# Optimization experiments

Measured on AMD Instinct MI355X. Metric: run time of the kernel, lower is better.

## Reference

```python
import jax, jax.numpy as jnp
import numpy as np

# pywt db4 decomposition filters (dec_lo, dec_hi), length 8
DB4_DEC_LO = np.array([-0.010597401784997278, 0.032883011666982945,
                       0.030841381835986965, -0.18703481171888114,
                       -0.02798376941698385, 0.6308807679295904,
                       0.7148465705525415, 0.23037781330885523], dtype=np.float32)
DB4_DEC_HI = np.array([-0.23037781330885523, 0.7148465705525415,
                       -0.6308807679295904, -0.02798376941698385,
                       0.18703481171888114, 0.030841381835986965,
                       -0.032883011666982945, -0.010597401784997278], dtype=np.float32)
LEVEL = 3


def setup_inputs() -> dict:
    key = jax.random.key(0)
    x = jax.random.normal(key, (64, 32, 4096), dtype=jnp.float32)  # (B, N, T)
    return {"x": x,
            "dec_lo": jnp.asarray(DB4_DEC_LO),
            "dec_hi": jnp.asarray(DB4_DEC_HI)}


def _swt(x, dec_lo, dec_hi, level=LEVEL):
    """Stationary (a trous) wavelet transform, matching ptwt.swt semantics."""
    B, N, T = x.shape
    filt_len = dec_lo.shape[0]
    # ptwt flips the filters so conv1d (correlation) performs true convolution
    filt = jnp.stack([dec_lo[::-1], dec_hi[::-1]], axis=0)[:, None, :]  # (2, 1, L)
    res_lo = x.reshape(B * N, 1, T)
    details = []
    for lvl in range(level):
        dil = 2 ** lvl
        padl = dil * (filt_len // 2 - 1)
        padr = dil * (filt_len // 2)
        padded = jnp.pad(res_lo, ((0, 0), (0, 0), (padl, padr)), mode="wrap")  # circular
        res = jax.lax.conv_general_dilated(
            padded, filt, window_strides=(1,), padding="VALID",
            rhs_dilation=(dil,), dimension_numbers=("NCH", "OIH", "NCH"))  # (BN, 2, T)
        res_lo = res[:, 0:1, :]
        details.append(res[:, 1, :])
    # ptwt ordering: [cA_level, cD_level, ..., cD_1]
    coeffs = [res_lo[:, 0, :]] + details[::-1]
    stacked = jnp.stack(coeffs, axis=1)  # (B*N, level+1, T)
    return stacked.reshape(B, N, level + 1, T).transpose(0, 1, 3, 2)  # (B, N, T, level+1)


def reference(x, dec_lo, dec_hi):
    return _swt(x, dec_lo, dec_hi)
```

## Files before the change

### kernel.cpp

```cpp
#include <hip/hip_runtime.h>

#define TLEN 4096
#define NT 256
#define SEG 1024
#define OFF 24
#define BUFW 1088

typedef float f32x4 __attribute__((ext_vector_type(4)));
typedef float f32x2 __attribute__((ext_vector_type(2)));

__device__ __forceinline__ f32x4 ldv4(const float* p) {
    return *reinterpret_cast<const f32x4*>(p);
}

#define W16(n) ((n) < 4 ? qa[(n)] : (n) < 8 ? qb[(n)-4] : (n) < 12 ? qc[(n)-8] : qd[(n)-12])
#define W20(n) ((n) < 4 ? qa[(n)] : (n) < 8 ? qb[(n)-4] : (n) < 12 ? qc[(n)-8] : (n) < 16 ? qd[(n)-12] : qe[(n)-16])
#define W32(n) ((n) < 4 ? qa[(n)] : (n) < 8 ? qb[(n)-4] : (n) < 12 ? qc[(n)-8] : (n) < 16 ? qd[(n)-12] : \
                (n) < 20 ? qe[(n)-16] : (n) < 24 ? qf[(n)-20] : (n) < 28 ? qg[(n)-24] : qh[(n)-28])

__global__ __launch_bounds__(NT) void swt_db4_l3_kernel(
    const float* __restrict__ x,
    const float* __restrict__ lo_g,
    const float* __restrict__ hi_g,
    float* __restrict__ out)
{
    __shared__ float bufX[BUFW];
    __shared__ float bufY[BUFW];
    __shared__ float pl[4][SEG];

    const int bid = blockIdx.x;
    const int row = bid >> 2;
    const int seg = (bid & 3) << 10;
    const int tid = threadIdx.x;

    f32x2 c[8];
#pragma unroll
    for (int j = 0; j < 8; ++j) { c[j].x = lo_g[j]; c[j].y = hi_g[j]; }

    const float* xr = x + (size_t)row * TLEN;

    {
        int idx = 4 * tid;
        *reinterpret_cast<f32x4*>(&bufX[OFF + idx]) = ldv4(xr + seg + idx);
    }
    if (tid < 49) {
        int u = (tid < 21) ? (tid - 21) : (SEG + tid - 21);
        bufX[OFF + u] = xr[(seg + u) & (TLEN - 1)];
    }
    __syncthreads();

    float d1[4], d2[4], a3[4], d3[4];

    {
        const float* b = &bufX[OFF + 4 * tid - 4];
        f32x4 qa = ldv4(b), qb = ldv4(b + 4), qc = ldv4(b + 8), qd = ldv4(b + 12);
        f32x2 acc[4];
#pragma unroll
        for (int i = 0; i < 4; ++i) { acc[i].x = 0.f; acc[i].y = 0.f; }
#pragma unroll
        for (int j = 0; j < 8; ++j)
#pragma unroll
            for (int i = 0; i < 4; ++i) {
                float v = W16(i + 8 - j);
                f32x2 vv; vv.x = v; vv.y = v;
                acc[i] = __builtin_elementwise_fma(c[j], vv, acc[i]);
            }
        f32x4 av; av.x = acc[0].x; av.y = acc[1].x; av.z = acc[2].x; av.w = acc[3].x;
        *reinterpret_cast<f32x4*>(&bufY[OFF + 4 * tid]) = av;
#pragma unroll
        for (int i = 0; i < 4; ++i) d1[i] = acc[i].y;
    }
    if (tid < 42) {
        int u = (tid < 18) ? (tid - 18) : (SEG + tid - 18);
        const float* s = &bufX[OFF + u];
        float a = 0.f;
#pragma unroll
        for (int j = 0; j < 8; ++j) a = fmaf(c[j].x, s[4 - j], a);
        bufY[OFF + u] = a;
    }
    __syncthreads();

    {
        const float* b = &bufY[OFF + 4 * tid - 8];
        f32x4 qa = ldv4(b), qb = ldv4(b + 4), qc = ldv4(b + 8), qd = ldv4(b + 12), qe = ldv4(b + 16);
        f32x2 acc[4];
#pragma unroll
        for (int i = 0; i < 4; ++i) { acc[i].x = 0.f; acc[i].y = 0.f; }
#pragma unroll
        for (int j = 0; j < 8; ++j)
#pragma unroll
            for (int i = 0; i < 4; ++i) {
                float v = W20(i + 16 - 2 * j);
                f32x2 vv; vv.x = v; vv.y = v;
                acc[i] = __builtin_elementwise_fma(c[j], vv, acc[i]);
            }
        f32x4 av; av.x = acc[0].x; av.y = acc[1].x; av.z = acc[2].x; av.w = acc[3].x;
        *reinterpret_cast<f32x4*>(&bufX[OFF + 4 * tid]) = av;
#pragma unroll
        for (int i = 0; i < 4; ++i) d2[i] = acc[i].y;
    }
    if (tid < 28) {
        int u = (tid < 12) ? (tid - 12) : (SEG + tid - 12);
        const float* s = &bufY[OFF + u];
        float a = 0.f;
#pragma unroll
        for (int j = 0; j < 8; ++j) a = fmaf(c[j].x, s[(4 - j) * 2], a);
        bufX[OFF + u] = a;
    }
    __syncthreads();

    {
        const float* b = &bufX[OFF + 4 * tid - 12];
        f32x4 qa = ldv4(b),      qb = ldv4(b + 4),  qc = ldv4(b + 8),  qd = ldv4(b + 12),
              qe = ldv4(b + 16), qf = ldv4(b + 20), qg = ldv4(b + 24), qh = ldv4(b + 28);
        f32x2 acc[4];
#pragma unroll
        for (int i = 0; i < 4; ++i) { acc[i].x = 0.f; acc[i].y = 0.f; }
#pragma unroll
        for (int j = 0; j < 8; ++j)
#pragma unroll
            for (int i = 0; i < 4; ++i) {
                float v = W32(i + 28 - 4 * j);
                f32x2 vv; vv.x = v; vv.y = v;
                acc[i] = __builtin_elementwise_fma(c[j], vv, acc[i]);
            }
#pragma unroll
        for (int i = 0; i < 4; ++i) { a3[i] = acc[i].x; d3[i] = acc[i].y; }
    }

    {
        f32x4 v0, v1, v2, v3;
        v0.x=a3[0]; v0.y=a3[1]; v0.z=a3[2]; v0.w=a3[3];
        v1.x=d3[0]; v1.y=d3[1]; v1.z=d3[2]; v1.w=d3[3];
        v2.x=d2[0]; v2.y=d2[1]; v2.z=d2[2]; v2.w=d2[3];
        v3.x=d1[0]; v3.y=d1[1]; v3.z=d1[2]; v3.w=d1[3];
        *reinterpret_cast<f32x4*>(&pl[0][4 * tid]) = v0;
        *reinterpret_cast<f32x4*>(&pl[1][4 * tid]) = v1;
        *reinterpret_cast<f32x4*>(&pl[2][4 * tid]) = v2;
        *reinterpret_cast<f32x4*>(&pl[3][4 * tid]) = v3;
    }
    __syncthreads();

    f32x4* outr = reinterpret_cast<f32x4*>(out + (size_t)row * TLEN * 4) + seg;
#pragma unroll
    for (int k = 0; k < 4; ++k) {
        int t = tid + k * NT;
        f32x4 o;
        o.x = pl[0][t];
        o.y = pl[1][t];
        o.z = pl[2][t];
        o.w = pl[3][t];
        outr[t] = o;
    }
}

extern "C" void kernel_launch(void* const* d_in, const int* in_sizes, int n_in,
                              void* d_out, int out_size, void* d_ws, size_t ws_size,
                              hipStream_t stream) {
    const float* x  = (const float*)d_in[0];
    const float* lo = (const float*)d_in[1];
    const float* hi = (const float*)d_in[2];
    float* out = (float*)d_out;

    const int nblocks = 64 * 32 * 4;
    swt_db4_l3_kernel<<<dim3(nblocks), dim3(NT), 0, stream>>>(x, lo, hi, out);
}
```

Measured before the change: 31.56 us.

## Process all four segments per block with prefetch of next segment's input

Each block now handles a whole row, looping over four 1024-sample segments instead of launching one block per segment. The global load for the next segment is issued before the current segment's compute so its latency overlaps the convolution work, and the shared buffers are merged so the output staging area aliases the work buffers. The intent is to hide global-load latency and reduce block launch overhead. The cost is a quarter as many blocks, which lowers parallelism, plus extra barriers per segment that serialize the stages within a block.

```diff
diff --git a/kernel.cpp b/kernel.cpp
--- a/kernel.cpp
+++ b/kernel.cpp
@@ -4,7 +4,8 @@
 #define NT 256
 #define SEG 1024
 #define OFF 24
-#define BUFW 1088
+#define BUFW 2176
+#define NSEGS 4
 
 typedef float f32x4 __attribute__((ext_vector_type(4)));
 typedef float f32x2 __attribute__((ext_vector_type(2)));
@@ -24,13 +25,12 @@
     const float* __restrict__ hi_g,
     float* __restrict__ out)
 {
-    __shared__ float bufX[BUFW];
-    __shared__ float bufY[BUFW];
-    __shared__ float pl[4][SEG];
+    __shared__ float lds[2 * BUFW];
+    float* bufX = lds;
+    float* bufY = lds + BUFW;
+    float* pl   = lds;
 
-    const int bid = blockIdx.x;
-    const int row = bid >> 2;
-    const int seg = (bid & 3) << 10;
+    const int row = blockIdx.x;
     const int tid = threadIdx.x;
 
     f32x2 c[8];
@@ -38,119 +38,133 @@
     for (int j = 0; j < 8; ++j) { c[j].x = lo_g[j]; c[j].y = hi_g[j]; }
 
     const float* xr = x + (size_t)row * TLEN;
+    f32x4* outb = reinterpret_cast<f32x4*>(out + (size_t)row * TLEN * 4);
 
-    {
-        int idx = 4 * tid;
-        *reinterpret_cast<f32x4*>(&bufX[OFF + idx]) = ldv4(xr + seg + idx);
-    }
-    if (tid < 49) {
-        int u = (tid < 21) ? (tid - 21) : (SEG + tid - 21);
-        bufX[OFF + u] = xr[(seg + u) & (TLEN - 1)];
-    }
-    __syncthreads();
+    const int hu = (tid < 21) ? (tid - 21) : (SEG + tid - 21);
 
-    float d1[4], d2[4], a3[4], d3[4];
+    f32x4 xpre = ldv4(xr + 4 * tid);
+    float xh = (tid < 49) ? xr[hu & (TLEN - 1)] : 0.f;
 
-    {
-        const float* b = &bufX[OFF + 4 * tid - 4];
-        f32x4 qa = ldv4(b), qb = ldv4(b + 4), qc = ldv4(b + 8), qd = ldv4(b + 12);
-        f32x2 acc[4];
+    for (int s = 0; s < NSEGS; ++s) {
+        *reinterpret_cast<f32x4*>(&bufX[OFF + 4 * tid]) = xpre;
+        if (tid < 49) bufX[OFF + hu] = xh;
+        __syncthreads();
+
+        f32x4 xnext;
+        float xhn = 0.f;
+        if (s + 1 < NSEGS) {
+            xnext = ldv4(xr + (s + 1) * SEG + 4 * tid);
+            if (tid < 49) xhn = xr[((s + 1) * SEG + hu) & (TLEN - 1)];
+        }
+
+        float d1[4], d2[4], a3[4], d3[4];
+
+        {
+            const float* b = &bufX[OFF + 4 * tid - 4];
+            f32x4 qa = ldv4(b), qb = ldv4(b + 4), qc = ldv4(b + 8), qd = ldv4(b + 12);
+            f32x2 acc[4];
 #pragma unroll
-        for (int i = 0; i < 4; ++i) { acc[i].x = 0.f; acc[i].y = 0.f; }
+            for (int i = 0; i < 4; ++i) { acc[i].x = 0.f; acc[i].y = 0.f; }
 #pragma unroll
-        for (int j = 0; j < 8; ++j)
+            for (int j = 0; j < 8; ++j)
 #pragma unroll
-            for (int i = 0; i < 4; ++i) {
-                float v = W16(i + 8 - j);
-                f32x2 vv; vv.x = v; vv.y = v;
-                acc[i] = __builtin_elementwise_fma(c[j], vv, acc[i]);
-            }
-        f32x4 av; av.x = acc[0].x; av.y = acc[1].x; av.z = acc[2].x; av.w = acc[3].x;
-        *reinterpret_cast<f32x4*>(&bufY[OFF + 4 * tid]) = av;
+                for (int i = 0; i < 4; ++i) {
+                    float v = W16(i + 8 - j);
+                    f32x2 vv; vv.x = v; vv.y = v;
+                    acc[i] = __builtin_elementwise_fma(c[j], vv, acc[i]);
+                }
+            f32x4 av; av.x = acc[0].x; av.y = acc[1].x; av.z = acc[2].x; av.w = acc[3].x;
+            *reinterpret_cast<f32x4*>(&bufY[OFF + 4 * tid]) = av;
 #pragma unroll
-        for (int i = 0; i < 4; ++i) d1[i] = acc[i].y;
-    }
-    if (tid < 42) {
-        int u = (tid < 18) ? (tid - 18) : (SEG + tid - 18);
-        const float* s = &bufX[OFF + u];
-        float a = 0.f;
+            for (int i = 0; i < 4; ++i) d1[i] = acc[i].y;
+        }
+        if (tid < 42) {
+            int u = (tid < 18) ? (tid - 18) : (SEG + tid - 18);
+            const float* sp = &bufX[OFF + u];
+            float a = 0.f;
 #pragma unroll
-        for (int j = 0; j < 8; ++j) a = fmaf(c[j].x, s[4 - j], a);
-        bufY[OFF + u] = a;
-    }
-    __syncthreads();
+            for (int j = 0; j < 8; ++j) a = fmaf(c[j].x, sp[4 - j], a);
+            bufY[OFF + u] = a;
+        }
+        __syncthreads();
 
-    {
-        const float* b = &bufY[OFF + 4 * tid - 8];
-        f32x4 qa = ldv4(b), qb = ldv4(b + 4), qc = ldv4(b + 8), qd = ldv4(b + 12), qe = ldv4(b + 16);
-        f32x2 acc[4];
+        {
+            const float* b = &bufY[OFF + 4 * tid - 8];
+            f32x4 qa = ldv4(b), qb = ldv4(b + 4), qc = ldv4(b + 8), qd = ldv4(b + 12), qe = ldv4(b + 16);
+            f32x2 acc[4];
 #pragma unroll
-        for (int i = 0; i < 4; ++i) { acc[i].x = 0.f; acc[i].y = 0.f; }
+            for (int i = 0; i < 4; ++i) { acc[i].x = 0.f; acc[i].y = 0.f; }
 #pragma unroll
-        for (int j = 0; j < 8; ++j)
+            for (int j = 0; j < 8; ++j)
 #pragma unroll
-            for (int i = 0; i < 4; ++i) {
-                float v = W20(i + 16 - 2 * j);
-                f32x2 vv; vv.x = v; vv.y = v;
-                acc[i] = __builtin_elementwise_fma(c[j], vv, acc[i]);
-            }
-        f32x4 av; av.x = acc[0].x; av.y = acc[1].x; av.z = acc[2].x; av.w = acc[3].x;
-        *reinterpret_cast<f32x4*>(&bufX[OFF + 4 * tid]) = av;
+                for (int i = 0; i < 4; ++i) {
+                    float v = W20(i + 16 - 2 * j);
+                    f32x2 vv; vv.x = v; vv.y = v;
+                    acc[i] = __builtin_elementwise_fma(c[j], vv, acc[i]);
+                }
+            f32x4 av; av.x = acc[0].x; av.y = acc[1].x; av.z = acc[2].x; av.w = acc[3].x;
+            *reinterpret_cast<f32x4*>(&bufX[OFF + 4 * tid]) = av;
 #pragma unroll
-        for (int i = 0; i < 4; ++i) d2[i] = acc[i].y;
-    }
-    if (tid < 28) {
-        int u = (tid < 12) ? (tid - 12) : (SEG + tid - 12);
-        const float* s = &bufY[OFF + u];
-        float a = 0.f;
+            for (int i = 0; i < 4; ++i) d2[i] = acc[i].y;
+        }
+        if (tid < 28) {
+            int u = (tid < 12) ? (tid - 12) : (SEG + tid - 12);
+            const float* sp = &bufY[OFF + u];
+            float a = 0.f;
 #pragma unroll
-        for (int j = 0; j < 8; ++j) a = fmaf(c[j].x, s[(4 - j) * 2], a);
-        bufX[OFF + u] = a;
-    }
-    __syncthreads();
+            for (int j = 0; j < 8; ++j) a = fmaf(c[j].x, sp[(4 - j) * 2], a);
+            bufX[OFF + u] = a;
+        }
+        __syncthreads();
 
-    {
-        const float* b = &bufX[OFF + 4 * tid - 12];
-        f32x4 qa = ldv4(b),      qb = ldv4(b + 4),  qc = ldv4(b + 8),  qd = ldv4(b + 12),
-              qe = ldv4(b + 16), qf = ldv4(b + 20), qg = ldv4(b + 24), qh = ldv4(b + 28);
-        f32x2 acc[4];
+        {
+            const float* b = &bufX[OFF + 4 * tid - 12];
+            f32x4 qa = ldv4(b),      qb = ldv4(b + 4),  qc = ldv4(b + 8),  qd = ldv4(b + 12),
+                  qe = ldv4(b + 16), qf = ldv4(b + 20), qg = ldv4(b + 24), qh = ldv4(b + 28);
+            f32x2 acc[4];
 #pragma unroll
-        for (int i = 0; i < 4; ++i) { acc[i].x = 0.f; acc[i].y = 0.f; }
+            for (int i = 0; i < 4; ++i) { acc[i].x = 0.f; acc[i].y = 0.f; }
 #pragma unroll
-        for (int j = 0; j < 8; ++j)
+            for (int j = 0; j < 8; ++j)
 #pragma unroll
-            for (int i = 0; i < 4; ++i) {
-                float v = W32(i + 28 - 4 * j);
-                f32x2 vv; vv.x = v; vv.y = v;
-                acc[i] = __builtin_elementwise_fma(c[j], vv, acc[i]);
-            }
+                for (int i = 0; i < 4; ++i) {
+                    float v = W32(i + 28 - 4 * j);
+                    f32x2 vv; vv.x = v; vv.y = v;
+                    acc[i] = __builtin_elementwise_fma(c[j], vv, acc[i]);
+                }
 #pragma unroll
-        for (int i = 0; i < 4; ++i) { a3[i] = acc[i].x; d3[i] = acc[i].y; }
-    }
+            for (int i = 0; i < 4; ++i) { a3[i] = acc[i].x; d3[i] = acc[i].y; }
+        }
+        __syncthreads();
 
-    {
-        f32x4 v0, v1, v2, v3;
-        v0.x=a3[0]; v0.y=a3[1]; v0.z=a3[2]; v0.w=a3[3];
-        v1.x=d3[0]; v1.y=d3[1]; v1.z=d3[2]; v1.w=d3[3];
-        v2.x=d2[0]; v2.y=d2[1]; v2.z=d2[2]; v2.w=d2[3];
-        v3.x=d1[0]; v3.y=d1[1]; v3.z=d1[2]; v3.w=d1[3];
-        *reinterpret_cast<f32x4*>(&pl[0][4 * tid]) = v0;
-        *reinterpret_cast<f32x4*>(&pl[1][4 * tid]) = v1;
-        *reinterpret_cast<f32x4*>(&pl[2][4 * tid]) = v2;
-        *reinterpret_cast<f32x4*>(&pl[3][4 * tid]) = v3;
-    }
-    __syncthreads();
+        {
+            f32x4 v0, v1, v2, v3;
+            v0.x=a3[0]; v0.y=a3[1]; v0.z=a3[2]; v0.w=a3[3];
+            v1.x=d3[0]; v1.y=d3[1]; v1.z=d3[2]; v1.w=d3[3];
+            v2.x=d2[0]; v2.y=d2[1]; v2.z=d2[2]; v2.w=d2[3];
+            v3.x=d1[0]; v3.y=d1[1]; v3.z=d1[2]; v3.w=d1[3];
+            *reinterpret_cast<f32x4*>(&pl[0 * SEG + 4 * tid]) = v0;
+            *reinterpret_cast<f32x4*>(&pl[1 * SEG + 4 * tid]) = v1;
+            *reinterpret_cast<f32x4*>(&pl[2 * SEG + 4 * tid]) = v2;
+            *reinterpret_cast<f32x4*>(&pl[3 * SEG + 4 * tid]) = v3;
+        }
+        __syncthreads();
 
-    f32x4* outr = reinterpret_cast<f32x4*>(out + (size_t)row * TLEN * 4) + seg;
+        f32x4* outr = outb + s * SEG;
 #pragma unroll
-    for (int k = 0; k < 4; ++k) {
-        int t = tid + k * NT;
-        f32x4 o;
-        o.x = pl[0][t];
-        o.y = pl[1][t];
-        o.z = pl[2][t];
-        o.w = pl[3][t];
-        outr[t] = o;
+        for (int k = 0; k < 4; ++k) {
+            int t = tid + k * NT;
+            f32x4 o;
+            o.x = pl[0 * SEG + t];
+            o.y = pl[1 * SEG + t];
+            o.z = pl[2 * SEG + t];
+            o.w = pl[3 * SEG + t];
+            outr[t] = o;
+        }
+        __syncthreads();
+
+        xpre = xnext;
+        xh = xhn;
     }
 }
 
@@ -162,6 +176,6 @@
     const float* hi = (const float*)d_in[2];
     float* out = (float*)d_out;
 
-    const int nblocks = 64 * 32 * 4;
+    const int nblocks = 64 * 32;
     swt_db4_l3_kernel<<<dim3(nblocks), dim3(NT), 0, stream>>>(x, lo, hi, out);
 }
```

Result: no change. 31.77 us (+0.7%).
